# Performance work log

Measured on AMD Instinct MI355X. Metric: run time of the kernel, lower is better.

The kernel has to match this reference:

```python
import jax, jax.numpy as jnp
import numpy as np

N = 50000   # num nodes
E = 800000  # num edges (avg degree 16)
L = 4       # num_blocks
H = 128     # hidden_dim
CD = 3      # coords_dim
VD = 3      # vel_dim
FD = 16     # node feature dim = node_dim - coords_dim - vel_dim
ED = 16     # edge_dim
DIN = 2 * H + ED + 1  # edge MLP input dim = 273


def setup_inputs() -> dict:
    key = jax.random.key(0)
    ks = jax.random.split(key, 32)
    s = 0.05
    inp = {}
    inp['nodes'] = jax.random.normal(ks[0], (N, CD + VD + FD), jnp.float32)
    # avoid self-loops (start==end) so the coord-diff norm is never exactly 0
    start = jax.random.randint(ks[1], (E,), 0, N)
    off = jax.random.randint(ks[2], (E,), 1, N)
    inp['edge_indices'] = jnp.stack([start, (start + off) % N]).astype(jnp.int64)
    inp['edge_features'] = jax.random.normal(ks[3], (E, ED), jnp.float32)
    # node embedding
    inp['emb_w'] = (jax.random.normal(ks[4], (FD, H)) * s).astype(jnp.float32)
    inp['emb_b'] = jnp.zeros((H,), jnp.float32)
    # per-block params, stacked over L blocks
    def w(k, shape):
        return (jax.random.normal(k, shape) * s).astype(jnp.float32)
    inp['ew1'] = w(ks[5], (L, DIN, H)); inp['eb1'] = jnp.zeros((L, H), jnp.float32)
    inp['ew2'] = w(ks[6], (L, H, H));   inp['eb2'] = jnp.zeros((L, H), jnp.float32)
    inp['cw1'] = w(ks[7], (L, H, H));   inp['cb1'] = jnp.zeros((L, H), jnp.float32)
    inp['cw2'] = w(ks[8], (L, H, CD));  inp['cb2'] = jnp.zeros((L, CD), jnp.float32)
    inp['vw1'] = w(ks[9], (L, H, H));   inp['vb1'] = jnp.zeros((L, H), jnp.float32)
    inp['vw2'] = w(ks[10], (L, H, 1));  inp['vb2'] = jnp.zeros((L, 1), jnp.float32)
    inp['nw1'] = w(ks[11], (L, 2 * H, H)); inp['nb1'] = jnp.zeros((L, H), jnp.float32)
    inp['nw2'] = w(ks[12], (L, H, H));  inp['nb2'] = jnp.zeros((L, H), jnp.float32)
    return inp


def _forward(nodes, edge_features, emb_w, emb_b, ew1, eb1, ew2, eb2,
             cw1, cb1, cw2, cb2, vw1, vb1, vw2, vb2, nw1, nb1, nw2, nb2,
             edge_indices):
    silu = jax.nn.silu
    coords = nodes[:, :CD]
    vels = nodes[:, CD:CD + VD]
    h = nodes[:, CD + VD:] @ emb_w + emb_b  # [N, H]
    start, end = edge_indices[0], edge_indices[1]
    n = coords.shape[0]
    # per-node edge counts for the coordinate mean-aggregation
    cnt = jax.ops.segment_sum(jnp.ones((start.shape[0], 1), coords.dtype),
                              start, num_segments=n)
    cnt = jnp.maximum(cnt, 1.0)
    for l in range(L):
        cd = coords[start] - coords[end]                       # [E, CD]
        nrm = jnp.sqrt(jnp.sum(cd * cd, axis=1, keepdims=True))  # [E, 1]
        x = jnp.concatenate([h[start], h[end], nrm, edge_features], axis=1)
        m = silu(silu(x @ ew1[l] + eb1[l]) @ ew2[l] + eb2[l])  # [E, H]
        # coordinate update: mean-aggregated weighted diffs + velocity term
        ct = cd * (silu(m @ cw1[l] + cb1[l]) @ cw2[l] + cb2[l])
        coords = coords + jax.ops.segment_sum(ct, start, num_segments=n) / cnt
        coords = coords + (silu(h @ vw1[l] + vb1[l]) @ vw2[l] + vb2[l]) * vels
        # node update: sum-aggregated messages
        agg = jax.ops.segment_sum(m, start, num_segments=n)    # [N, H]
        h = h + silu(jnp.concatenate([h, agg], axis=1) @ nw1[l] + nb1[l]) @ nw2[l] + nb2[l]
    return coords  # prediction_type == 'coords'


def reference(nodes, edge_indices, edge_features, emb_w, emb_b,
              ew1, eb1, ew2, eb2, cw1, cb1, cw2, cb2,
              vw1, vb1, vw2, vb2, nw1, nb1, nw2, nb2):
    return _forward(nodes, edge_features, emb_w, emb_b, ew1, eb1, ew2, eb2,
                    cw1, cb1, cw2, cb2, vw1, vb1, vw2, vb2,
                    nw1, nb1, nw2, nb2, edge_indices)
```

## Files before the change

kernel.cpp:

```cpp
#include <hip/hip_runtime.h>

constexpr int NN = 50000;
constexpr int EE = 800000;
constexpr int HH = 128;

typedef __attribute__((ext_vector_type(8))) __bf16 bfv8;
typedef __attribute__((ext_vector_type(4))) float f32x4;
typedef unsigned short u16;

__device__ __forceinline__ u16 f2bf(float x){
  unsigned u = __builtin_bit_cast(unsigned, x);
  u = u + 0x7fffu + ((u >> 16) & 1u);
  return (u16)(u >> 16);
}
__device__ __forceinline__ float fsilu(float x){ return x / (1.f + __expf(-x)); }

template<int KSTEPS, int CB, int RB>
__device__ __forceinline__ void mm_tile(const u16* A, int Rbase, const u16* __restrict__ Bp,
                                        const float* __restrict__ bias, int NB, f32x4* acc){
  const int lane = threadIdx.x & 63;
  #pragma unroll
  for (int cb = 0; cb < CB; ++cb){
    int col = cb*16 + (lane & 15);
    float b = (col < NB) ? bias[col] : 0.f;
    acc[cb] = (f32x4){b, b, b, b};
  }
  const int arow = Rbase + (lane & 15);
  const char* abase = (const char*)A + arow * RB;
  const int kb = (lane >> 4) * 16;
  const int swz = (arow & 7) << 4;
  const bfv8* __restrict__ bq = (const bfv8*)Bp + lane;
  for (int ks = 0; ks < KSTEPS; ++ks){
    bfv8 a = *(const bfv8*)(abase + ((ks*64 + kb) ^ swz));
    #pragma unroll
    for (int cb = 0; cb < CB; ++cb){
      bfv8 b = bq[(ks*CB + cb) * 64];
      acc[cb] = __builtin_amdgcn_mfma_f32_16x16x32_bf16(a, b, acc[cb], 0, 0, 0);
    }
  }
}

template<int CB>
__device__ __forceinline__ void silu_store(const f32x4* acc, u16* dst, int Rbase){
  const int lane = threadIdx.x & 63;
  #pragma unroll
  for (int cb = 0; cb < CB; ++cb){
    #pragma unroll
    for (int j = 0; j < 4; ++j){
      int row = Rbase + ((lane >> 4) << 2) + j;
      int col = cb*16 + (lane & 15);
      float s = fsilu(acc[cb][j]);
      *(u16*)((char*)dst + row*256 + ((col*2) ^ ((row & 7) << 4))) = f2bf(s);
    }
  }
}

struct PackDesc { const float* src; u16* dst; int K; int Nc; int CB; int ksteps; };
struct PackArgs { PackDesc d[32]; };

__global__ __launch_bounds__(256) void pack_kernel(PackArgs pa){
  PackDesc d = pa.d[blockIdx.x];
  int total = d.ksteps * d.CB * 512;
  for (int p = threadIdx.x; p < total; p += 256){
    int j = p & 7, lane = (p >> 3) & 63, cbk = p >> 9;
    int cb = cbk % d.CB, ks = cbk / d.CB;
    int k = ks*32 + ((lane >> 4) * 8) + j;
    int col = cb*16 + (lane & 15);
    float v = (k < d.K && col < d.Nc) ? d.src[(size_t)k * d.Nc + col] : 0.f;
    d.dst[p] = f2bf(v);
  }
}

__global__ __launch_bounds__(256) void embed_kernel(const float* __restrict__ nodes,
    const float* __restrict__ emb_w, const float* __restrict__ emb_b,
    float* __restrict__ hf, u16* __restrict__ hbf, float* __restrict__ coords){
  int t = blockIdx.x * 256 + threadIdx.x;
  int g = t >> 2, q = t & 3;
  if (g >= NN) return;
  const float* x = nodes + (size_t)g * 22;
  float acc[32];
  #pragma unroll
  for (int c = 0; c < 32; ++c) acc[c] = emb_b[q*32 + c];
  for (int k = 0; k < 16; ++k){
    float f = x[6 + k];
    const float* wr = emb_w + k*128 + q*32;
    #pragma unroll
    for (int c = 0; c < 32; ++c) acc[c] += f * wr[c];
  }
  size_t off = (size_t)g * HH + q*32;
  #pragma unroll
  for (int c = 0; c < 32; ++c){ hf[off + c] = acc[c]; hbf[off + c] = f2bf(acc[c]); }
  if (q == 0){
    coords[g*3+0] = x[0]; coords[g*3+1] = x[1]; coords[g*3+2] = x[2];
  }
}

__global__ __launch_bounds__(256) void cnt_kernel(const int* __restrict__ esrc, float* __restrict__ cnt){
  int e = blockIdx.x * 256 + threadIdx.x;
  if (e < EE) atomicAdd(&cnt[esrc[e]], 1.f);
}

__global__ __launch_bounds__(256) void edge_kernel(
    const float* __restrict__ coords, const u16* __restrict__ hbf, const float* __restrict__ ef,
    const int* __restrict__ esrc, const int* __restrict__ edst,
    const u16* __restrict__ ew1p, const u16* __restrict__ ew2p,
    const u16* __restrict__ cw1p, const u16* __restrict__ cw2p,
    const float* __restrict__ eb1, const float* __restrict__ eb2,
    const float* __restrict__ cb1, const float* __restrict__ cb2,
    float* __restrict__ agg, float* __restrict__ acc_ct){
  __shared__ u16 sX[64 * 320];
  __shared__ float4 s_cdn[64];
  __shared__ int s_src[64];
  __shared__ int s_dst[64];

  const int tid = threadIdx.x, wid = tid >> 6, lane = tid & 63;
  const int R = wid * 16;
  const int e0 = blockIdx.x * 64;

  if (lane < 16){
    int row = R + lane;
    int e = e0 + row;
    int s = esrc[e], d = edst[e];
    float cx = coords[s*3+0] - coords[d*3+0];
    float cy = coords[s*3+1] - coords[d*3+1];
    float cz = coords[s*3+2] - coords[d*3+2];
    float nrm = sqrtf(cx*cx + cy*cy + cz*cz);
    s_cdn[row] = make_float4(cx, cy, cz, nrm);
    s_src[row] = s; s_dst[row] = d;
  }
  {
    int row = R + (lane >> 2), q = lane & 3;
    int e = e0 + row;
    int s = s_src[row], d = s_dst[row];
    const uint4* hs = (const uint4*)(hbf + (size_t)s * HH);
    const uint4* hd = (const uint4*)(hbf + (size_t)d * HH);
    float4 cdn = s_cdn[row];
    #pragma unroll
    for (int c = 0; c < 9; ++c){
      int col8 = q*72 + c*8;
      uint4 v;
      if (col8 < 128) v = hs[col8 >> 3];
      else if (col8 < 256) v = hd[(col8 - 128) >> 3];
      else {
        float f[8];
        #pragma unroll
        for (int j = 0; j < 8; ++j){
          int gk = col8 - 256 + j;
          float x = 0.f;
          if (gk == 0) x = cdn.w;
          else if (gk <= 16) x = ef[(size_t)e * 16 + (gk - 1)];
          f[j] = x;
        }
        v.x = f2bf(f[0]) | ((unsigned)f2bf(f[1]) << 16);
        v.y = f2bf(f[2]) | ((unsigned)f2bf(f[3]) << 16);
        v.z = f2bf(f[4]) | ((unsigned)f2bf(f[5]) << 16);
        v.w = f2bf(f[6]) | ((unsigned)f2bf(f[7]) << 16);
      }
      *(uint4*)((char*)sX + row*640 + ((col8*2) ^ ((row & 7) << 4))) = v;
    }
  }

  f32x4 acc[8];
  mm_tile<9, 8, 640>(sX, R, ew1p, eb1, 128, acc);
  __syncthreads();
  u16* M1 = sX;
  u16* Mb = sX + 8192;
  silu_store<8>(acc, M1, R);

  mm_tile<4, 8, 256>(M1, R, ew2p, eb2, 128, acc);
  {
    int rbase = R + ((lane >> 4) << 2);
    int sidx[4];
    #pragma unroll
    for (int j = 0; j < 4; ++j) sidx[j] = s_src[rbase + j];
    #pragma unroll
    for (int cb = 0; cb < 8; ++cb){
      int col = cb*16 + (lane & 15);
      #pragma unroll
      for (int j = 0; j < 4; ++j){
        int row = rbase + j;
        float m = fsilu(acc[cb][j]);
        atomicAdd(&agg[(size_t)sidx[j] * HH + col], m);
        *(u16*)((char*)Mb + row*256 + ((col*2) ^ ((row & 7) << 4))) = f2bf(m);
      }
    }
  }

  mm_tile<4, 8, 256>(Mb, R, cw1p, cb1, 128, acc);
  silu_store<8>(acc, M1, R);

  f32x4 a4[1];
  mm_tile<4, 1, 256>(M1, R, cw2p, cb2, 3, a4);
  {
    int col = lane & 15;
    if (col < 3){
      #pragma unroll
      for (int j = 0; j < 4; ++j){
        int row = R + ((lane >> 4) << 2) + j;
        float4 cdn = s_cdn[row];
        float cdv = (col == 0) ? cdn.x : ((col == 1) ? cdn.y : cdn.z);
        atomicAdd(&acc_ct[(size_t)s_src[row] * 3 + col], cdv * a4[0][j]);
      }
    }
  }
}

__global__ __launch_bounds__(256) void node_kernel(
    float* __restrict__ coords, float* __restrict__ hf, u16* __restrict__ hbf,
    const float* __restrict__ agg, const float* __restrict__ acc_ct, const float* __restrict__ cnt,
    const float* __restrict__ nodes,
    const u16* __restrict__ vw1p, const u16* __restrict__ vw2p,
    const u16* __restrict__ nw1p, const u16* __restrict__ nw2p,
    const float* __restrict__ vb1, const float* __restrict__ vb2,
    const float* __restrict__ nb1, const float* __restrict__ nb2){
  __shared__ u16 sXn[64 * 256];
  __shared__ u16 sV[64 * 128];
  __shared__ float s_vt[64];

  const int tid = threadIdx.x, wid = tid >> 6, lane = tid & 63;
  const int R = wid * 16;
  const int g0 = blockIdx.x * 64;

  {
    int row = R + (lane >> 2), q = lane & 3, g = g0 + row;
    #pragma unroll
    for (int c = 0; c < 8; ++c){
      int col8 = q*64 + c*8;
      uint4 v = {0, 0, 0, 0};
      if (g < NN){
        if (col8 < 128) v = ((const uint4*)(hbf + (size_t)g * HH))[col8 >> 3];
        else {
          const float* ap = agg + (size_t)g * HH + (col8 - 128);
          float4 a0 = *(const float4*)ap;
          float4 a1 = *(const float4*)(ap + 4);
          v.x = f2bf(a0.x) | ((unsigned)f2bf(a0.y) << 16);
          v.y = f2bf(a0.z) | ((unsigned)f2bf(a0.w) << 16);
          v.z = f2bf(a1.x) | ((unsigned)f2bf(a1.y) << 16);
          v.w = f2bf(a1.z) | ((unsigned)f2bf(a1.w) << 16);
        }
      }
      *(uint4*)((char*)sXn + row*512 + ((col8*2) ^ ((row & 7) << 4))) = v;
    }
  }

  f32x4 acc[8];
  mm_tile<4, 8, 512>(sXn, R, vw1p, vb1, 128, acc);
  silu_store<8>(acc, sV, R);
  f32x4 a1[1];
  mm_tile<4, 1, 256>(sV, R, vw2p, vb2, 1, a1);
  if ((lane & 15) == 0){
    #pragma unroll
    for (int j = 0; j < 4; ++j) s_vt[R + ((lane >> 4) << 2) + j] = a1[0][j];
  }
  if (lane < 16){
    int row = R + lane, g = g0 + row;
    if (g < NN){
      float cn = cnt[g]; cn = (cn < 1.f) ? 1.f : cn;
      float vt = s_vt[row];
      #pragma unroll
      for (int c = 0; c < 3; ++c){
        float val = coords[g*3 + c] + acc_ct[g*3 + c] / cn + vt * nodes[(size_t)g*22 + 3 + c];
        coords[g*3 + c] = val;
      }
    }
  }

  mm_tile<8, 8, 512>(sXn, R, nw1p, nb1, 128, acc);
  silu_store<8>(acc, sV, R);
  mm_tile<4, 8, 256>(sV, R, nw2p, nb2, 128, acc);
  {
    #pragma unroll
    for (int cb = 0; cb < 8; ++cb){
      int col = cb*16 + (lane & 15);
      #pragma unroll
      for (int j = 0; j < 4; ++j){
        int row = R + ((lane >> 4) << 2) + j, g = g0 + row;
        if (g < NN){
          size_t off = (size_t)g * HH + col;
          float h = acc[cb][j] + hf[off];
          hf[off] = h;
          hbf[off] = f2bf(h);
        }
      }
    }
  }
}

extern "C" void kernel_launch(void* const* d_in, const int* in_sizes, int n_in,
                              void* d_out, int out_size, void* d_ws, size_t ws_size,
                              hipStream_t stream){
  const float* nodes = (const float*)d_in[0];
  const int*   eidx  = (const int*)d_in[1];
  const float* ef    = (const float*)d_in[2];
  const float* emb_w = (const float*)d_in[3];
  const float* emb_b = (const float*)d_in[4];
  const float* ew1 = (const float*)d_in[5];
  const float* eb1 = (const float*)d_in[6];
  const float* ew2 = (const float*)d_in[7];
  const float* eb2 = (const float*)d_in[8];
  const float* cw1 = (const float*)d_in[9];
  const float* cb1 = (const float*)d_in[10];
  const float* cw2 = (const float*)d_in[11];
  const float* cb2 = (const float*)d_in[12];
  const float* vw1 = (const float*)d_in[13];
  const float* vb1 = (const float*)d_in[14];
  const float* vw2 = (const float*)d_in[15];
  const float* vb2 = (const float*)d_in[16];
  const float* nw1 = (const float*)d_in[17];
  const float* nb1 = (const float*)d_in[18];
  const float* nw2 = (const float*)d_in[19];
  const float* nb2 = (const float*)d_in[20];

  constexpr size_t WS_NEEDED = 70u * 1024u * 1024u;
  if (ws_size < WS_NEEDED) return;

  char* ws = (char*)d_ws;
  size_t off = 0;
  auto alloc = [&](size_t bytes){ void* p = ws + off; off += (bytes + 255) & ~(size_t)255; return p; };
  float* coords = (float*)alloc((size_t)NN * 3 * 4);
  float* hf     = (float*)alloc((size_t)NN * HH * 4);
  u16*   hbf    = (u16*)  alloc((size_t)NN * HH * 2);
  float* agg    = (float*)alloc((size_t)NN * 131 * 4);
  float* acc_ct = agg + (size_t)NN * HH;
  float* cnt    = (float*)alloc((size_t)NN * 4);

  constexpr int O_EW1 = 0;
  constexpr int O_EW2 = O_EW1 + 9*8*512;
  constexpr int O_CW1 = O_EW2 + 4*8*512;
  constexpr int O_CW2 = O_CW1 + 4*8*512;
  constexpr int O_VW1 = O_CW2 + 4*1*512;
  constexpr int O_VW2 = O_VW1 + 4*8*512;
  constexpr int O_NW1 = O_VW2 + 4*1*512;
  constexpr int O_NW2 = O_NW1 + 8*8*512;
  constexpr int LAYER_PACK = O_NW2 + 4*8*512;
  u16* packs = (u16*)alloc((size_t)LAYER_PACK * 4 * 2);

  PackArgs pa;
  for (int l = 0; l < 4; ++l){
    u16* base = packs + (size_t)l * LAYER_PACK;
    int i = l * 8;
    pa.d[i+0] = { ew1 + (size_t)l*273*128, base + O_EW1, 273, 128, 8, 9 };
    pa.d[i+1] = { ew2 + (size_t)l*128*128, base + O_EW2, 128, 128, 8, 4 };
    pa.d[i+2] = { cw1 + (size_t)l*128*128, base + O_CW1, 128, 128, 8, 4 };
    pa.d[i+3] = { cw2 + (size_t)l*128*3,   base + O_CW2, 128,   3, 1, 4 };
    pa.d[i+4] = { vw1 + (size_t)l*128*128, base + O_VW1, 128, 128, 8, 4 };
    pa.d[i+5] = { vw2 + (size_t)l*128*1,   base + O_VW2, 128,   1, 1, 4 };
    pa.d[i+6] = { nw1 + (size_t)l*256*128, base + O_NW1, 256, 128, 8, 8 };
    pa.d[i+7] = { nw2 + (size_t)l*128*128, base + O_NW2, 128, 128, 8, 4 };
  }

  pack_kernel<<<32, 256, 0, stream>>>(pa);
  embed_kernel<<<(NN*4 + 255)/256, 256, 0, stream>>>(nodes, emb_w, emb_b, hf, hbf, coords);
  hipMemsetAsync(cnt, 0, (size_t)NN * 4, stream);
  cnt_kernel<<<(EE + 255)/256, 256, 0, stream>>>(eidx, cnt);

  for (int l = 0; l < 4; ++l){
    hipMemsetAsync(agg, 0, (size_t)NN * 131 * 4, stream);
    u16* base = packs + (size_t)l * LAYER_PACK;
    edge_kernel<<<EE/64, 256, 0, stream>>>(coords, hbf, ef, eidx, eidx + EE,
        base + O_EW1, base + O_EW2, base + O_CW1, base + O_CW2,
        eb1 + l*128, eb2 + l*128, cb1 + l*128, cb2 + l*3, agg, acc_ct);
    node_kernel<<<(NN + 63)/64, 256, 0, stream>>>(coords, hf, hbf, agg, acc_ct, cnt, nodes,
        base + O_VW1, base + O_VW2, base + O_NW1, base + O_NW2,
        vb1 + l*128, vb2 + l, nb1 + l*128, nb2 + l*128);
  }

  hipMemcpyAsync(d_out, coords, (size_t)NN * 3 * 4, hipMemcpyDeviceToDevice, stream);
}
```

Baseline: 2.310 ms.

## Sort edges by source via CSR and pre-reduce segment atomics in registers

Builds a CSR ordering of edges by source node with count, scan and scatter kernels, then runs the edge kernel over sorted edges. Consecutive rows that share a source are summed in registers before one atomicAdd per run, which cuts atomic traffic to agg and acc_ct. The ew1 packing is remapped so edge features come before the norm, and each wave now uses its own scratch region, which removes a block barrier. It adds one-time sort kernels, a single-block serial scan, and an indirect read of edge features through the permuted edge ids.

```diff
diff --git a/kernel.cpp b/kernel.cpp
--- a/kernel.cpp
+++ b/kernel.cpp
@@ -55,7 +55,7 @@
   }
 }
 
-struct PackDesc { const float* src; u16* dst; int K; int Nc; int CB; int ksteps; };
+struct PackDesc { const float* src; u16* dst; int K; int Nc; int CB; int ksteps; int remap; };
 struct PackArgs { PackDesc d[32]; };
 
 __global__ __launch_bounds__(256) void pack_kernel(PackArgs pa){
@@ -66,7 +66,9 @@
     int cb = cbk % d.CB, ks = cbk / d.CB;
     int k = ks*32 + ((lane >> 4) * 8) + j;
     int col = cb*16 + (lane & 15);
-    float v = (k < d.K && col < d.Nc) ? d.src[(size_t)k * d.Nc + col] : 0.f;
+    int kk = k;
+    if (d.remap && k >= 256) kk = (k < 272) ? (k + 1) : ((k == 272) ? 256 : 0x7fffffff);
+    float v = (kk < d.K && col < d.Nc) ? d.src[(size_t)kk * d.Nc + col] : 0.f;
     d.dst[p] = f2bf(v);
   }
 }
@@ -95,14 +97,47 @@
   }
 }
 
-__global__ __launch_bounds__(256) void cnt_kernel(const int* __restrict__ esrc, float* __restrict__ cnt){
+__global__ __launch_bounds__(256) void count_kernel(const int* __restrict__ esrc, int* __restrict__ cnt_i){
   int e = blockIdx.x * 256 + threadIdx.x;
-  if (e < EE) atomicAdd(&cnt[esrc[e]], 1.f);
+  if (e < EE) atomicAdd(&cnt_i[esrc[e]], 1);
+}
+
+__global__ __launch_bounds__(256) void scan_kernel(const int* __restrict__ cnt_i,
+    int* __restrict__ row_start, int* __restrict__ fill){
+  __shared__ int part[256];
+  int t = threadIdx.x;
+  int lo = t * 196, hi = lo + 196;
+  if (lo > NN) lo = NN;
+  if (hi > NN) hi = NN;
+  int s = 0;
+  for (int i = lo; i < hi; ++i) s += cnt_i[i];
+  part[t] = s; __syncthreads();
+  for (int d = 1; d < 256; d <<= 1){
+    int v = (t >= d) ? part[t-d] : 0;
+    __syncthreads();
+    part[t] += v;
+    __syncthreads();
+  }
+  int run = part[t] - s;
+  for (int i = lo; i < hi; ++i){ row_start[i] = run; fill[i] = run; run += cnt_i[i]; }
+  if (t == 255) row_start[NN] = run;
+}
+
+__global__ __launch_bounds__(256) void scatter_kernel(const int* __restrict__ esrc,
+    const int* __restrict__ edst, int* __restrict__ fill,
+    int2* __restrict__ sd_sorted, int* __restrict__ eid_sorted){
+  int e = blockIdx.x * 256 + threadIdx.x;
+  if (e < EE){
+    int s = esrc[e];
+    int pos = atomicAdd(&fill[s], 1);
+    sd_sorted[pos] = make_int2(s, edst[e]);
+    eid_sorted[pos] = e;
+  }
 }
 
 __global__ __launch_bounds__(256) void edge_kernel(
     const float* __restrict__ coords, const u16* __restrict__ hbf, const float* __restrict__ ef,
-    const int* __restrict__ esrc, const int* __restrict__ edst,
+    const int2* __restrict__ sd_sorted, const int* __restrict__ eid_sorted,
     const u16* __restrict__ ew1p, const u16* __restrict__ ew2p,
     const u16* __restrict__ cw1p, const u16* __restrict__ cw2p,
     const float* __restrict__ eb1, const float* __restrict__ eb2,
@@ -112,6 +147,7 @@
   __shared__ float4 s_cdn[64];
   __shared__ int s_src[64];
   __shared__ int s_dst[64];
+  __shared__ int s_eid[64];
 
   const int tid = threadIdx.x, wid = tid >> 6, lane = tid & 63;
   const int R = wid * 16;
@@ -120,21 +156,21 @@
   if (lane < 16){
     int row = R + lane;
     int e = e0 + row;
-    int s = esrc[e], d = edst[e];
-    float cx = coords[s*3+0] - coords[d*3+0];
-    float cy = coords[s*3+1] - coords[d*3+1];
-    float cz = coords[s*3+2] - coords[d*3+2];
+    int2 sd = sd_sorted[e];
+    float cx = coords[sd.x*3+0] - coords[sd.y*3+0];
+    float cy = coords[sd.x*3+1] - coords[sd.y*3+1];
+    float cz = coords[sd.x*3+2] - coords[sd.y*3+2];
     float nrm = sqrtf(cx*cx + cy*cy + cz*cz);
     s_cdn[row] = make_float4(cx, cy, cz, nrm);
-    s_src[row] = s; s_dst[row] = d;
+    s_src[row] = sd.x; s_dst[row] = sd.y; s_eid[row] = eid_sorted[e];
   }
   {
     int row = R + (lane >> 2), q = lane & 3;
-    int e = e0 + row;
-    int s = s_src[row], d = s_dst[row];
+    int s = s_src[row], d = s_dst[row], eid = s_eid[row];
     const uint4* hs = (const uint4*)(hbf + (size_t)s * HH);
     const uint4* hd = (const uint4*)(hbf + (size_t)d * HH);
-    float4 cdn = s_cdn[row];
+    const float* efp = ef + (size_t)eid * 16;
+    float nrm = s_cdn[row].w;
     #pragma unroll
     for (int c = 0; c < 9; ++c){
       int col8 = q*72 + c*8;
@@ -146,10 +182,7 @@
         #pragma unroll
         for (int j = 0; j < 8; ++j){
           int gk = col8 - 256 + j;
-          float x = 0.f;
-          if (gk == 0) x = cdn.w;
-          else if (gk <= 16) x = ef[(size_t)e * 16 + (gk - 1)];
-          f[j] = x;
+          f[j] = (gk < 16) ? efp[gk] : ((gk == 16) ? nrm : 0.f);
         }
         v.x = f2bf(f[0]) | ((unsigned)f2bf(f[1]) << 16);
         v.y = f2bf(f[2]) | ((unsigned)f2bf(f[3]) << 16);
@@ -160,46 +193,63 @@
     }
   }
 
+  u16* wb = sX + R * 320;
+  u16* Mb = wb + 2048;
+
   f32x4 acc[8];
   mm_tile<9, 8, 640>(sX, R, ew1p, eb1, 128, acc);
-  __syncthreads();
-  u16* M1 = sX;
-  u16* Mb = sX + 8192;
-  silu_store<8>(acc, M1, R);
-
-  mm_tile<4, 8, 256>(M1, R, ew2p, eb2, 128, acc);
+  silu_store<8>(acc, wb, 0);
+
+  mm_tile<4, 8, 256>(wb, 0, ew2p, eb2, 128, acc);
   {
-    int rbase = R + ((lane >> 4) << 2);
-    int sidx[4];
-    #pragma unroll
-    for (int j = 0; j < 4; ++j) sidx[j] = s_src[rbase + j];
-    #pragma unroll
-    for (int cb = 0; cb < 8; ++cb){
-      int col = cb*16 + (lane & 15);
+    const int rb = (lane >> 4) << 2;
+    float run[8];
+    #pragma unroll
+    for (int cb = 0; cb < 8; ++cb) run[cb] = 0.f;
+    #pragma unroll
+    for (int j = 0; j < 4; ++j){
+      int grow = R + rb + j;
+      int src = s_src[grow];
+      bool flush = (j == 3) || (s_src[grow + 1] != src);
       #pragma unroll
-      for (int j = 0; j < 4; ++j){
-        int row = rbase + j;
+      for (int cb = 0; cb < 8; ++cb){
+        int col = cb*16 + (lane & 15);
         float m = fsilu(acc[cb][j]);
-        atomicAdd(&agg[(size_t)sidx[j] * HH + col], m);
-        *(u16*)((char*)Mb + row*256 + ((col*2) ^ ((row & 7) << 4))) = f2bf(m);
-      }
-    }
-  }
-
-  mm_tile<4, 8, 256>(Mb, R, cw1p, cb1, 128, acc);
-  silu_store<8>(acc, M1, R);
+        run[cb] += m;
+        *(u16*)((char*)Mb + (rb + j)*256 + ((col*2) ^ (((rb + j) & 7) << 4))) = f2bf(m);
+      }
+      if (flush){
+        #pragma unroll
+        for (int cb = 0; cb < 8; ++cb){
+          int col = cb*16 + (lane & 15);
+          atomicAdd(&agg[(size_t)src * HH + col], run[cb]);
+          run[cb] = 0.f;
+        }
+      }
+    }
+  }
+
+  mm_tile<4, 8, 256>(Mb, 0, cw1p, cb1, 128, acc);
+  silu_store<8>(acc, wb, 0);
 
   f32x4 a4[1];
-  mm_tile<4, 1, 256>(M1, R, cw2p, cb2, 3, a4);
+  mm_tile<4, 1, 256>(wb, 0, cw2p, cb2, 3, a4);
   {
     int col = lane & 15;
     if (col < 3){
+      const int rb = (lane >> 4) << 2;
+      float run = 0.f;
       #pragma unroll
       for (int j = 0; j < 4; ++j){
-        int row = R + ((lane >> 4) << 2) + j;
-        float4 cdn = s_cdn[row];
+        int grow = R + rb + j;
+        float4 cdn = s_cdn[grow];
         float cdv = (col == 0) ? cdn.x : ((col == 1) ? cdn.y : cdn.z);
-        atomicAdd(&acc_ct[(size_t)s_src[row] * 3 + col], cdv * a4[0][j]);
+        run += cdv * a4[0][j];
+        int src = s_src[grow];
+        if (j == 3 || s_src[grow + 1] != src){
+          atomicAdd(&acc_ct[(size_t)src * 3 + col], run);
+          run = 0.f;
+        }
       }
     }
   }
@@ -207,7 +257,7 @@
 
 __global__ __launch_bounds__(256) void node_kernel(
     float* __restrict__ coords, float* __restrict__ hf, u16* __restrict__ hbf,
-    const float* __restrict__ agg, const float* __restrict__ acc_ct, const float* __restrict__ cnt,
+    const float* __restrict__ agg, const float* __restrict__ acc_ct, const int* __restrict__ row_start,
     const float* __restrict__ nodes,
     const u16* __restrict__ vw1p, const u16* __restrict__ vw2p,
     const u16* __restrict__ nw1p, const u16* __restrict__ nw2p,
@@ -255,7 +305,8 @@
   if (lane < 16){
     int row = R + lane, g = g0 + row;
     if (g < NN){
-      float cn = cnt[g]; cn = (cn < 1.f) ? 1.f : cn;
+      float cn = (float)(row_start[g + 1] - row_start[g]);
+      if (cn < 1.f) cn = 1.f;
       float vt = s_vt[row];
       #pragma unroll
       for (int c = 0; c < 3; ++c){
@@ -311,18 +362,22 @@
   const float* nw2 = (const float*)d_in[19];
   const float* nb2 = (const float*)d_in[20];
 
-  constexpr size_t WS_NEEDED = 70u * 1024u * 1024u;
+  constexpr size_t WS_NEEDED = 78u * 1024u * 1024u;
   if (ws_size < WS_NEEDED) return;
 
   char* ws = (char*)d_ws;
   size_t off = 0;
   auto alloc = [&](size_t bytes){ void* p = ws + off; off += (bytes + 255) & ~(size_t)255; return p; };
-  float* coords = (float*)alloc((size_t)NN * 3 * 4);
-  float* hf     = (float*)alloc((size_t)NN * HH * 4);
-  u16*   hbf    = (u16*)  alloc((size_t)NN * HH * 2);
-  float* agg    = (float*)alloc((size_t)NN * 131 * 4);
-  float* acc_ct = agg + (size_t)NN * HH;
-  float* cnt    = (float*)alloc((size_t)NN * 4);
+  float* coords   = (float*)alloc((size_t)NN * 3 * 4);
+  float* hf       = (float*)alloc((size_t)NN * HH * 4);
+  u16*   hbf      = (u16*)  alloc((size_t)NN * HH * 2);
+  float* agg      = (float*)alloc((size_t)NN * 131 * 4);
+  float* acc_ct   = agg + (size_t)NN * HH;
+  int*   cnt_i    = (int*)  alloc((size_t)NN * 4);
+  int*   row_start= (int*)  alloc((size_t)(NN + 1) * 4);
+  int*   fill     = (int*)  alloc((size_t)NN * 4);
+  int2*  sd_sorted= (int2*) alloc((size_t)EE * 8);
+  int*   eid_sorted=(int*)  alloc((size_t)EE * 4);
 
   constexpr int O_EW1 = 0;
   constexpr int O_EW2 = O_EW1 + 9*8*512;
@@ -339,28 +394,30 @@
   for (int l = 0; l < 4; ++l){
     u16* base = packs + (size_t)l * LAYER_PACK;
     int i = l * 8;
-    pa.d[i+0] = { ew1 + (size_t)l*273*128, base + O_EW1, 273, 128, 8, 9 };
-    pa.d[i+1] = { ew2 + (size_t)l*128*128, base + O_EW2, 128, 128, 8, 4 };
-    pa.d[i+2] = { cw1 + (size_t)l*128*128, base + O_CW1, 128, 128, 8, 4 };
-    pa.d[i+3] = { cw2 + (size_t)l*128*3,   base + O_CW2, 128,   3, 1, 4 };
-    pa.d[i+4] = { vw1 + (size_t)l*128*128, base + O_VW1, 128, 128, 8, 4 };
-    pa.d[i+5] = { vw2 + (size_t)l*128*1,   base + O_VW2, 128,   1, 1, 4 };
-    pa.d[i+6] = { nw1 + (size_t)l*256*128, base + O_NW1, 256, 128, 8, 8 };
-    pa.d[i+7] = { nw2 + (size_t)l*128*128, base + O_NW2, 128, 128, 8, 4 };
+    pa.d[i+0] = { ew1 + (size_t)l*273*128, base + O_EW1, 273, 128, 8, 9, 1 };
+    pa.d[i+1] = { ew2 + (size_t)l*128*128, base + O_EW2, 128, 128, 8, 4, 0 };
+    pa.d[i+2] = { cw1 + (size_t)l*128*128, base + O_CW1, 128, 128, 8, 4, 0 };
+    pa.d[i+3] = { cw2 + (size_t)l*128*3,   base + O_CW2, 128,   3, 1, 4, 0 };
+    pa.d[i+4] = { vw1 + (size_t)l*128*128, base + O_VW1, 128, 128, 8, 4, 0 };
+    pa.d[i+5] = { vw2 + (size_t)l*128*1,   base + O_VW2, 128,   1, 1, 4, 0 };
+    pa.d[i+6] = { nw1 + (size_t)l*256*128, base + O_NW1, 256, 128, 8, 8, 0 };
+    pa.d[i+7] = { nw2 + (size_t)l*128*128, base + O_NW2, 128, 128, 8, 4, 0 };
   }
 
   pack_kernel<<<32, 256, 0, stream>>>(pa);
   embed_kernel<<<(NN*4 + 255)/256, 256, 0, stream>>>(nodes, emb_w, emb_b, hf, hbf, coords);
-  hipMemsetAsync(cnt, 0, (size_t)NN * 4, stream);
-  cnt_kernel<<<(EE + 255)/256, 256, 0, stream>>>(eidx, cnt);
+  hipMemsetAsync(cnt_i, 0, (size_t)NN * 4, stream);
+  count_kernel<<<(EE + 255)/256, 256, 0, stream>>>(eidx, cnt_i);
+  scan_kernel<<<1, 256, 0, stream>>>(cnt_i, row_start, fill);
+  scatter_kernel<<<(EE + 255)/256, 256, 0, stream>>>(eidx, eidx + EE, fill, sd_sorted, eid_sorted);
 
   for (int l = 0; l < 4; ++l){
     hipMemsetAsync(agg, 0, (size_t)NN * 131 * 4, stream);
     u16* base = packs + (size_t)l * LAYER_PACK;
-    edge_kernel<<<EE/64, 256, 0, stream>>>(coords, hbf, ef, eidx, eidx + EE,
+    edge_kernel<<<EE/64, 256, 0, stream>>>(coords, hbf, ef, sd_sorted, eid_sorted,
         base + O_EW1, base + O_EW2, base + O_CW1, base + O_CW2,
         eb1 + l*128, eb2 + l*128, cb1 + l*128, cb2 + l*3, agg, acc_ct);
-    node_kernel<<<(NN + 63)/64, 256, 0, stream>>>(coords, hf, hbf, agg, acc_ct, cnt, nodes,
+    node_kernel<<<(NN + 63)/64, 256, 0, stream>>>(coords, hf, hbf, agg, acc_ct, row_start, nodes,
         base + O_VW1, base + O_VW2, base + O_NW1, base + O_NW2,
         vb1 + l*128, vb2 + l, nb1 + l*128, nb2 + l*128);
   }
```

Result: slower. 2.405 ms (+4.1%).
